# Optimization experiments

Hardware: AMD Instinct MI355X
Metric: run time of the kernel (lower is better)

## Reference

```python
import jax, jax.numpy as jnp
import numpy as np

B, C, H, T = 16384, 4, 8, 120
DT = 10.0        # ms per step
THRESH = 0.5     # decision threshold (buffer, non-trainable)
ALPHA = 0.2      # state update rate


def setup_inputs() -> dict:
    key = jax.random.key(0)
    ks = jax.random.split(key, 7)
    comp = np.full((C, C), -0.05, dtype=np.float32)
    np.fill_diagonal(comp, 0.25)
    return {
        "logits": jax.random.normal(ks[0], (B, C), jnp.float32),
        "input_scale": jnp.float32(0.25),
        "noise_std": jnp.float32(0.02),
        "input_proj_w": jax.random.normal(ks[1], (H, 1), jnp.float32),   # Linear(1,H) weight
        "input_proj_b": jax.random.normal(ks[2], (H,), jnp.float32) * 0.1,
        "self_proj_w": jax.random.normal(ks[3], (H, H), jnp.float32) / np.sqrt(H),  # Linear(H,H,bias=False)
        "comp_proj_w": jax.random.normal(ks[4], (H, 1), jnp.float32),   # Linear(1,H,bias=False)
        "evidence_w": jax.random.normal(ks[5], (1, H), jnp.float32) / np.sqrt(H),   # Linear(H,1) weight
        "evidence_b": jnp.zeros((1,), jnp.float32),
        "class_bias": jnp.zeros((C, H), jnp.float32),
        "competition": jnp.asarray(comp),
        # pre-drawn standard-normal noise for all T steps (torch draws randn per step)
        "noise": jax.random.normal(ks[6], (T, B, C, H), jnp.float32),
    }


def _rollout(logits, input_scale, noise_std, input_proj_w, input_proj_b,
             self_proj_w, comp_proj_w, evidence_w, evidence_b,
             class_bias, competition, noise):
    # input embed: relu(logits*scale)[...,None] @ input_proj + class_bias  -> [B,C,H]
    inp = (jax.nn.relu(logits * input_scale)[:, :, None] * input_proj_w[:, 0]
           + input_proj_b + class_bias[None])
    ev_w, ev_b = evidence_w[0], evidence_b[0]

    def step(state, noise_t):
        ev = jnp.einsum('bch,h->bc', state, ev_w) + ev_b          # evidence_head(state)
        comp = ev @ competition                                   # [B,C]
        cand = jnp.tanh(jnp.einsum('bch,kh->bck', state, self_proj_w)
                        + inp
                        + comp[:, :, None] * comp_proj_w[:, 0]
                        + noise_t * noise_std)
        new_state = state + ALPHA * (cand - state)
        new_ev = jnp.einsum('bch,h->bc', new_state, ev_w) + ev_b
        return new_state, (new_ev, new_ev - ev)

    state0 = jnp.zeros((logits.shape[0], C, H), logits.dtype)
    _, (ev_traj, dsdt_traj) = jax.lax.scan(step, state0, noise)
    # [T,B,C] -> [B,T,C]
    return jnp.transpose(ev_traj, (1, 0, 2)), jnp.transpose(dsdt_traj, (1, 0, 2))


def _decision_times(x):
    # first time index where (evidence - threshold) > 0, else never-crossed -> T*dt
    crossed = x > 0                      # [B,T,C]
    any_c = jnp.any(crossed, axis=1)     # [B,C]
    idx = jnp.argmax(crossed, axis=1)    # [B,C] first crossing step
    return jnp.where(any_c, (idx + 1).astype(jnp.float32) * DT,
                     jnp.float32(T * DT))


def reference(logits, input_scale, noise_std, input_proj_w, input_proj_b,
              self_proj_w, comp_proj_w, evidence_w, evidence_b,
              class_bias, competition, noise):
    ev_traj, _ = _rollout(logits, input_scale, noise_std, input_proj_w,
                          input_proj_b, self_proj_w, comp_proj_w,
                          evidence_w, evidence_b, class_bias, competition, noise)
    return _decision_times(ev_traj - THRESH) / 1000.0
```

## Files before the change

### kernel.cpp

```cpp
#include <hip/hip_runtime.h>

namespace {

constexpr int kB = 16384;
constexpr int kC = 4;
constexpr int kH = 8;
constexpr int kT = 120;
constexpr float kAlpha  = 0.2f;
constexpr float kDT     = 10.0f;
constexpr float kThresh = 0.5f;
constexpr float kNever  = (float)kT * kDT;

__device__ __forceinline__ float fast_tanh(float x) {
    float e = __expf(x + x);
    float r = __builtin_amdgcn_rcpf(e + 1.0f);
    return fmaf(-2.0f, r, 1.0f);
}

template <int CTRL>
__device__ __forceinline__ float qperm(float x) {
    return __builtin_bit_cast(float, __builtin_amdgcn_mov_dpp(
        __builtin_bit_cast(int, x), CTRL, 0xF, 0xF, true));
}

__global__ __launch_bounds__(256) void acc_rnn_kernel(
    const float* __restrict__ logits,
    const float* __restrict__ p_iscale,
    const float* __restrict__ p_nstd,
    const float* __restrict__ ipw_,
    const float* __restrict__ ipb_,
    const float* __restrict__ spw_,
    const float* __restrict__ cpw_,
    const float* __restrict__ evw_,
    const float* __restrict__ evb_,
    const float* __restrict__ cbias_,
    const float* __restrict__ compmat_,
    const float* __restrict__ noise_,
    float* __restrict__ out)
{
    const int tid = blockIdx.x * 256 + threadIdx.x;
    const int c   = tid & (kC - 1);

    const float iscale = p_iscale[0];
    const float nstd   = p_nstd[0];
    const float evb    = evb_[0];

    float W[kH][kH], cpw[kH], evw[kH];
#pragma unroll
    for (int k = 0; k < kH; ++k) {
        cpw[k] = cpw_[k];
        evw[k] = evw_[k];
#pragma unroll
        for (int h = 0; h < kH; ++h) W[k][h] = spw_[k * kH + h];
    }

    const float mw0 = compmat_[(c ^ 0) * kC + c];
    const float mw1 = compmat_[(c ^ 1) * kC + c];
    const float mw2 = compmat_[(c ^ 2) * kC + c];
    const float mw3 = compmat_[(c ^ 3) * kC + c];

    float rl = logits[tid] * iscale;
    rl = rl > 0.0f ? rl : 0.0f;
    float inp[kH];
#pragma unroll
    for (int k = 0; k < kH; ++k)
        inp[k] = fmaf(rl, ipw_[k], ipb_[k] + cbias_[c * kH + k]);

    float s[kH];
#pragma unroll
    for (int k = 0; k < kH; ++k) s[k] = 0.0f;
    float ev = evb;

    const float4* np4 = (const float4*)noise_;
    const int stepStride = kB * kC * kH / 4;
    const int lane = tid * 2;

    float4 nb[6][2];
#pragma unroll
    for (int j = 0; j < 6; ++j) {
        nb[j][0] = np4[j * stepStride + lane];
        nb[j][1] = np4[j * stepStride + lane + 1];
    }

    float tdec = kNever;
    float tcf  = 0.0f;

    auto do_step = [&](int t, int j, bool PF) {
        float e1 = qperm<0xB1>(ev);
        float e2 = qperm<0x4E>(ev);
        float e3 = qperm<0x1B>(ev);
        float comp = fmaf(e1, mw1, ev * mw0) + fmaf(e3, mw3, e2 * mw2);

        float nz[kH] = {nb[j][0].x, nb[j][0].y, nb[j][0].z, nb[j][0].w,
                        nb[j][1].x, nb[j][1].y, nb[j][1].z, nb[j][1].w};

        if (PF) {
            nb[j][0] = np4[(t + 6) * stepStride + lane];
            nb[j][1] = np4[(t + 6) * stepStride + lane + 1];
        }

        float cand[kH];
#pragma unroll
        for (int k = 0; k < kH; ++k) {
            float a = fmaf(comp, cpw[k], inp[k]);
            a = fmaf(nz[k], nstd, a);
#pragma unroll
            for (int h = 0; h < kH; ++h) a = fmaf(s[h], W[k][h], a);
            cand[k] = fast_tanh(a);
        }

        float nev = evb;
#pragma unroll
        for (int k = 0; k < kH; ++k) {
            s[k] = fmaf(kAlpha, cand[k] - s[k], s[k]);
            nev = fmaf(s[k], evw[k], nev);
        }
        ev = nev;

        tcf += kDT;
        tdec = fminf(tdec, ev > kThresh ? tcf : kNever);
    };

    for (int t0 = 0; t0 < kT - 6; t0 += 6) {
#pragma unroll
        for (int j = 0; j < 6; ++j) do_step(t0 + j, j, true);
    }
#pragma unroll
    for (int j = 0; j < 6; ++j) do_step(kT - 6 + j, j, false);

    out[tid] = tdec * (1.0f / 1000.0f);
}

}

extern "C" void kernel_launch(void* const* d_in, const int* in_sizes, int n_in,
                              void* d_out, int out_size, void* d_ws, size_t ws_size,
                              hipStream_t stream) {
    (void)in_sizes; (void)n_in; (void)d_ws; (void)ws_size; (void)out_size;
    const float* logits   = (const float*)d_in[0];
    const float* iscale   = (const float*)d_in[1];
    const float* nstd     = (const float*)d_in[2];
    const float* ipw      = (const float*)d_in[3];
    const float* ipb      = (const float*)d_in[4];
    const float* spw      = (const float*)d_in[5];
    const float* cpw      = (const float*)d_in[6];
    const float* evw      = (const float*)d_in[7];
    const float* evb      = (const float*)d_in[8];
    const float* cbias    = (const float*)d_in[9];
    const float* compmat  = (const float*)d_in[10];
    const float* noise    = (const float*)d_in[11];
    float* out = (float*)d_out;

    dim3 grid(kB * kC / 256), block(256);
    acc_rnn_kernel<<<grid, block, 0, stream>>>(
        logits, iscale, nstd, ipw, ipb, spw, cpw, evw, evb,
        cbias, compmat, noise, out);
}
```

Before: 357.2 us.

## Split hidden dimension across two lanes per (batch,class) using DPP exchanges

Each (batch,class) pair is now handled by two threads, each owning four of the eight hidden units. The other half's state comes in through DPP lane moves (xor-4), and the evidence partial sums are combined the same way. Doubling the thread count raises parallelism and latency hiding for the serial 120-step recurrence and halves per-thread registers, at the cost of extra cross-lane moves each step. Noise loads also switch to nontemporal float4 loads.

```diff
diff --git a/kernel.cpp b/kernel.cpp
--- a/kernel.cpp
+++ b/kernel.cpp
@@ -11,6 +11,8 @@
 constexpr float kThresh = 0.5f;
 constexpr float kNever  = (float)kT * kDT;
 
+typedef float vf4 __attribute__((ext_vector_type(4)));
+
 __device__ __forceinline__ float fast_tanh(float x) {
     float e = __expf(x + x);
     float r = __builtin_amdgcn_rcpf(e + 1.0f);
@@ -18,9 +20,12 @@
 }
 
 template <int CTRL>
-__device__ __forceinline__ float qperm(float x) {
+__device__ __forceinline__ float dppmov(float x) {
     return __builtin_bit_cast(float, __builtin_amdgcn_mov_dpp(
         __builtin_bit_cast(int, x), CTRL, 0xF, 0xF, true));
+}
+__device__ __forceinline__ float xor4(float x) {
+    return dppmov<0x1B>(dppmov<0x141>(x));
 }
 
 __global__ __launch_bounds__(256) void acc_rnn_kernel(
@@ -38,20 +43,27 @@
     const float* __restrict__ noise_,
     float* __restrict__ out)
 {
-    const int tid = blockIdx.x * 256 + threadIdx.x;
-    const int c   = tid & (kC - 1);
+    const int tid  = blockIdx.x * 256 + threadIdx.x;
+    const int c    = tid & 3;
+    const int half = (tid >> 2) & 1;
+    const int kOfs = half << 2;
+    const int pid  = ((tid >> 3) << 2) | c;
 
     const float iscale = p_iscale[0];
     const float nstd   = p_nstd[0];
     const float evb    = evb_[0];
 
-    float W[kH][kH], cpw[kH], evw[kH];
+    float Wown[4][4], Woth[4][4], cpw[4], evw[4];
 #pragma unroll
-    for (int k = 0; k < kH; ++k) {
-        cpw[k] = cpw_[k];
-        evw[k] = evw_[k];
+    for (int i = 0; i < 4; ++i) {
+        const int k = kOfs + i;
+        cpw[i] = cpw_[k];
+        evw[i] = evw_[k];
 #pragma unroll
-        for (int h = 0; h < kH; ++h) W[k][h] = spw_[k * kH + h];
+        for (int j = 0; j < 4; ++j) {
+            Wown[i][j] = spw_[k * kH + kOfs + j];
+            Woth[i][j] = spw_[k * kH + (kOfs ^ 4) + j];
+        }
     }
 
     const float mw0 = compmat_[(c ^ 0) * kC + c];
@@ -59,63 +71,61 @@
     const float mw2 = compmat_[(c ^ 2) * kC + c];
     const float mw3 = compmat_[(c ^ 3) * kC + c];
 
-    float rl = logits[tid] * iscale;
+    float rl = logits[pid] * iscale;
     rl = rl > 0.0f ? rl : 0.0f;
-    float inp[kH];
+    float inp[4];
 #pragma unroll
-    for (int k = 0; k < kH; ++k)
-        inp[k] = fmaf(rl, ipw_[k], ipb_[k] + cbias_[c * kH + k]);
+    for (int i = 0; i < 4; ++i)
+        inp[i] = fmaf(rl, ipw_[kOfs + i], ipb_[kOfs + i] + cbias_[c * kH + kOfs + i]);
 
-    float s[kH];
-#pragma unroll
-    for (int k = 0; k < kH; ++k) s[k] = 0.0f;
+    float s[4] = {0.0f, 0.0f, 0.0f, 0.0f};
     float ev = evb;
 
-    const float4* np4 = (const float4*)noise_;
+    const vf4* np4 = (const vf4*)noise_;
     const int stepStride = kB * kC * kH / 4;
-    const int lane = tid * 2;
+    const int base = (tid & ~7) + ((tid & 3) << 1) + half;
 
-    float4 nb[6][2];
+    vf4 nb[6];
 #pragma unroll
-    for (int j = 0; j < 6; ++j) {
-        nb[j][0] = np4[j * stepStride + lane];
-        nb[j][1] = np4[j * stepStride + lane + 1];
-    }
+    for (int j = 0; j < 6; ++j)
+        nb[j] = __builtin_nontemporal_load(&np4[j * stepStride + base]);
 
     float tdec = kNever;
     float tcf  = 0.0f;
 
     auto do_step = [&](int t, int j, bool PF) {
-        float e1 = qperm<0xB1>(ev);
-        float e2 = qperm<0x4E>(ev);
-        float e3 = qperm<0x1B>(ev);
+        float e1 = dppmov<0xB1>(ev);
+        float e2 = dppmov<0x4E>(ev);
+        float e3 = dppmov<0x1B>(ev);
         float comp = fmaf(e1, mw1, ev * mw0) + fmaf(e3, mw3, e2 * mw2);
 
-        float nz[kH] = {nb[j][0].x, nb[j][0].y, nb[j][0].z, nb[j][0].w,
-                        nb[j][1].x, nb[j][1].y, nb[j][1].z, nb[j][1].w};
+        float nz[4] = {nb[j].x, nb[j].y, nb[j].z, nb[j].w};
+        if (PF)
+            nb[j] = __builtin_nontemporal_load(&np4[(t + 6) * stepStride + base]);
 
-        if (PF) {
-            nb[j][0] = np4[(t + 6) * stepStride + lane];
-            nb[j][1] = np4[(t + 6) * stepStride + lane + 1];
+        float so[4];
+#pragma unroll
+        for (int i = 0; i < 4; ++i) so[i] = xor4(s[i]);
+
+        float cand[4];
+#pragma unroll
+        for (int i = 0; i < 4; ++i) {
+            float a = fmaf(comp, cpw[i], inp[i]);
+            a = fmaf(nz[i], nstd, a);
+#pragma unroll
+            for (int j2 = 0; j2 < 4; ++j2) a = fmaf(s[j2],  Wown[i][j2], a);
+#pragma unroll
+            for (int j2 = 0; j2 < 4; ++j2) a = fmaf(so[j2], Woth[i][j2], a);
+            cand[i] = fast_tanh(a);
         }
 
-        float cand[kH];
+        float evp = 0.0f;
 #pragma unroll
-        for (int k = 0; k < kH; ++k) {
-            float a = fmaf(comp, cpw[k], inp[k]);
-            a = fmaf(nz[k], nstd, a);
-#pragma unroll
-            for (int h = 0; h < kH; ++h) a = fmaf(s[h], W[k][h], a);
-            cand[k] = fast_tanh(a);
+        for (int i = 0; i < 4; ++i) {
+            s[i] = fmaf(kAlpha, cand[i] - s[i], s[i]);
+            evp = fmaf(s[i], evw[i], evp);
         }
-
-        float nev = evb;
-#pragma unroll
-        for (int k = 0; k < kH; ++k) {
-            s[k] = fmaf(kAlpha, cand[k] - s[k], s[k]);
-            nev = fmaf(s[k], evw[k], nev);
-        }
-        ev = nev;
+        ev = (evp + xor4(evp)) + evb;
 
         tcf += kDT;
         tdec = fminf(tdec, ev > kThresh ? tcf : kNever);
@@ -128,7 +138,7 @@
 #pragma unroll
     for (int j = 0; j < 6; ++j) do_step(kT - 6 + j, j, false);
 
-    out[tid] = tdec * (1.0f / 1000.0f);
+    if (half == 0) out[pid] = tdec * (1.0f / 1000.0f);
 }
 
 }
@@ -151,7 +161,7 @@
     const float* noise    = (const float*)d_in[11];
     float* out = (float*)d_out;
 
-    dim3 grid(kB * kC / 256), block(256);
+    dim3 grid(kB * kC * 2 / 256), block(256);
     acc_rnn_kernel<<<grid, block, 0, stream>>>(
         logits, iscale, nstd, ipw, ipb, spw, cpw, evw, evb,
         cbias, compmat, noise, out);
```

New measurement: 347.9 us. 2.6% less time.
